# Optimization experiments

Hardware: AMD Instinct MI355X
Metric: run time of the kernel (lower is better)

## Reference

```python
import jax, jax.numpy as jnp
import numpy as np
from jax import lax

NUM_CLASSES = 80
CONF_THRESH = 0.05
NMS_THRESH = 0.6
TOPK = 2000          # topk_results per FPN level
IMG = 1280           # square input image
STRIDES = (8, 16, 32)
CLASS_OFFSET = 1.0e4 # > max box coordinate, for class-aware NMS offset trick


def setup_inputs() -> dict:
    key = jax.random.key(0)
    ks = jax.random.split(key, 6)
    inp = {}
    for i, s in enumerate(STRIDES):
        hw = (IMG // s) ** 2
        # classification logits; shift down so sigmoid scores are realistic
        inp[f"cls_p{i+3}"] = jax.random.normal(ks[i], (1, hw, NUM_CLASSES), jnp.float32) - 2.0
        # decoded boxes in absolute xyxy pixel coords
        u = jax.random.uniform(ks[i + 3], (1, hw, 4), jnp.float32)
        xy = u[..., :2] * (IMG - 260.0)
        wh = u[..., 2:] * 256.0 + 4.0
        inp[f"box_p{i+3}"] = jnp.concatenate([xy, xy + wh], axis=-1)
    inp["img_w"] = IMG
    inp["img_h"] = IMG
    return inp


def _box_iou(boxes):
    # boxes: [N,4] xyxy -> [N,N] IoU
    x1, y1, x2, y2 = boxes[:, 0], boxes[:, 1], boxes[:, 2], boxes[:, 3]
    area = jnp.maximum(x2 - x1, 0.0) * jnp.maximum(y2 - y1, 0.0)  # [N]
    lt = jnp.maximum(boxes[:, None, :2], boxes[None, :, :2])      # [N,N,2]
    rb = jnp.minimum(boxes[:, None, 2:], boxes[None, :, 2:])      # [N,N,2]
    wh = jnp.maximum(rb - lt, 0.0)
    inter = wh[..., 0] * wh[..., 1]
    union = area[:, None] + area[None, :] - inter
    return inter / jnp.maximum(union, 1e-9)


def _post_process(cls_list, box_list):
    all_scores, all_labels, all_boxes, all_valid = [], [], [], []
    for cls_i, box_i in zip(cls_list, box_list):
        cls0 = cls_i[0]                 # [HW, C]
        box0 = box_i[0]                 # [HW, 4]
        scores_flat = jax.nn.sigmoid(cls0).reshape(-1)      # [HW*C]
        k = min(TOPK, box0.shape[0])    # as in torch: min(topk_results, num_anchors)
        topk_scores, topk_idxs = lax.top_k(scores_flat, k)  # desc sort + take k
        valid = topk_scores > CONF_THRESH
        labels = topk_idxs % NUM_CLASSES
        anchor_idxs = topk_idxs // NUM_CLASSES
        all_scores.append(topk_scores)
        all_labels.append(labels)
        all_boxes.append(box0[anchor_idxs])
        all_valid.append(valid)
    scores = jnp.concatenate(all_scores)   # [N]
    labels = jnp.concatenate(all_labels)   # [N]
    boxes = jnp.concatenate(all_boxes)     # [N,4]
    valid = jnp.concatenate(all_valid)     # [N]

    # sort all candidates by score (invalid last)
    order = jnp.argsort(-jnp.where(valid, scores, -jnp.inf))
    scores, labels, boxes, valid = scores[order], labels[order], boxes[order], valid[order]

    # class-aware NMS (ca_nms=False): offset boxes per class so IoU across classes is 0
    off = labels.astype(boxes.dtype)[:, None] * CLASS_OFFSET
    iou = _box_iou(lax.stop_gradient(boxes + off))          # [N,N]

    n = scores.shape[0]
    idxr = jnp.arange(n)

    def body(i, st):
        keep, sup = st
        active = jnp.logical_not(sup[i])
        keep = keep.at[i].set(active)
        sup = sup | (active & (iou[i] > NMS_THRESH) & (idxr > i))
        return keep, sup

    keep, _ = lax.fori_loop(0, n, body, (jnp.zeros(n, bool), jnp.logical_not(valid)))
    return boxes, scores, labels, keep


def reference(cls_p3, cls_p4, cls_p5, box_p3, box_p4, box_p5, img_w, img_h):
    boxes, scores, labels, keep = _post_process(
        [cls_p3, cls_p4, cls_p5], [box_p3, box_p4, box_p5])
    scale = jnp.array([1.0 / img_w, 1.0 / img_h, 1.0 / img_w, 1.0 / img_h],
                      dtype=boxes.dtype)
    bboxes = jnp.clip(boxes * scale, 0.0, 1.0)
    # fixed-size padded result: `keep` marks the surviving detections
    return bboxes, scores, labels, keep
```

## Files before the change

### kernel.cpp

```cpp
#include <hip/hip_runtime.h>
#include <math.h>

#define L0T 2048000
#define L1T 512000
#define L2T 128000
#define LTOT 2688000
#define NTOT 5600
#define NW 88
#define NCB 2048
#define HB 128
#define CANDCAP 8192
#define LCHUNK 1024
#define GCHUNK 700
#define PAIRCAP 4096

__device__ __forceinline__ unsigned mkey(float f){
  unsigned u = __float_as_uint(f);
  return u ^ ((unsigned)(((int)u) >> 31) | 0x80000000u);
}

__global__ __launch_bounds__(256) void hist_blocks(const float* __restrict__ c0,
                                                   const float* __restrict__ c1,
                                                   const float* __restrict__ c2,
                                                   unsigned* __restrict__ blockHist){
  __shared__ unsigned lh[6 * NCB];
  for (int i = threadIdx.x; i < 6 * NCB; i += 256) lh[i] = 0;
  __syncthreads();
  int wv = threadIdx.x >> 6;
  unsigned* h0 = lh + wv * NCB;
  unsigned* h1 = lh + 4 * NCB;
  unsigned* h2 = lh + 5 * NCB;
  int g = blockIdx.x * 256 + threadIdx.x;
  const int Q = LTOT / 4;
  for (int q = g; q < Q; q += HB * 256){
    int e = q * 4;
    int idx; const float* p; unsigned* h;
    if (e < L0T){ idx = e; p = c0; h = h0; }
    else if (e < L0T + L1T){ idx = e - L0T; p = c1; h = h1; }
    else { idx = e - (L0T + L1T); p = c2; h = h2; }
    float4 v = *(const float4*)(p + idx);
    atomicAdd(&h[mkey(v.x) >> 21], 1u);
    atomicAdd(&h[mkey(v.y) >> 21], 1u);
    atomicAdd(&h[mkey(v.z) >> 21], 1u);
    atomicAdd(&h[mkey(v.w) >> 21], 1u);
  }
  __syncthreads();
  unsigned* out = blockHist + (size_t)blockIdx.x * 3 * NCB;
  for (int i = threadIdx.x; i < 3 * NCB; i += 256){
    unsigned s;
    if (i < NCB)            s = lh[i] + lh[NCB + i] + lh[2 * NCB + i] + lh[3 * NCB + i];
    else if (i < 2 * NCB)   s = lh[4 * NCB + (i - NCB)];
    else                    s = lh[5 * NCB + (i - 2 * NCB)];
    out[i] = s;
  }
}

__global__ __launch_bounds__(256) void reduce_hist24(const unsigned* __restrict__ blockHist,
                                                     unsigned* __restrict__ ghist){
  int c = blockIdx.x * 256 + threadIdx.x;
  unsigned s = 0;
#pragma unroll 8
  for (int b = 0; b < HB; ++b) s += blockHist[(size_t)b * 3 * NCB + c];
  ghist[c] = s;
}

__global__ __launch_bounds__(256) void threshbase_kernel(const unsigned* __restrict__ ghist,
                                                         const unsigned* __restrict__ blockHist,
                                                         unsigned* __restrict__ T,
                                                         unsigned* __restrict__ blockBase,
                                                         unsigned* __restrict__ candCnt){
  __shared__ unsigned h[NCB];
  __shared__ unsigned sT;
  __shared__ unsigned cb[HB];
  int lvl = blockIdx.x;
  for (int c = threadIdx.x; c < NCB; c += 256) h[c] = ghist[lvl * NCB + c];
  __syncthreads();
  if (threadIdx.x < 64){
    int lane = threadIdx.x;
    unsigned K = (lvl == 2) ? 1600u : 2000u;
    unsigned p = 0;
    for (int b = lane * 32; b < lane * 32 + 32; ++b) p += h[b];
    unsigned sincl = p;
    for (int d = 1; d < 64; d <<= 1){
      unsigned t = __shfl_down(sincl, d);
      if (lane + d < 64) sincl += t;
    }
    unsigned s_after = sincl - p;
    if (s_after < K && s_after + p >= K){
      unsigned acc = s_after;
      for (int b = lane * 32 + 31; b >= lane * 32; --b){
        acc += h[b];
        if (acc >= K){ sT = (unsigned)b; break; }
      }
    }
  }
  __syncthreads();
  unsigned tt = sT;
  if (threadIdx.x == 0) T[lvl] = tt;
  if (threadIdx.x < HB){
    const unsigned* bh = blockHist + (size_t)threadIdx.x * 3 * NCB + lvl * NCB;
    unsigned s = 0;
    for (unsigned c = tt; c < NCB; ++c) s += bh[c];
    cb[threadIdx.x] = s;
  }
  __syncthreads();
  if (threadIdx.x == 0){
    unsigned acc = 0;
    for (int b = 0; b < HB; ++b){ unsigned v = cb[b]; blockBase[lvl * HB + b] = acc; acc += v; }
    candCnt[lvl] = (acc > CANDCAP) ? CANDCAP : acc;
  }
}

__global__ __launch_bounds__(256) void compact_kernel(const float* __restrict__ c0,
                                                      const float* __restrict__ c1,
                                                      const float* __restrict__ c2,
                                                      const unsigned* __restrict__ T,
                                                      const unsigned* __restrict__ blockBase,
                                                      unsigned long long* __restrict__ cand){
  __shared__ unsigned run[3];
  if (threadIdx.x < 3) run[threadIdx.x] = 0;
  __syncthreads();
  unsigned t0 = T[0], t1 = T[1], t2 = T[2];
  unsigned bb0 = blockBase[0 * HB + blockIdx.x];
  unsigned bb1 = blockBase[1 * HB + blockIdx.x];
  unsigned bb2 = blockBase[2 * HB + blockIdx.x];
  int lane = threadIdx.x & 63;
  unsigned long long ltmask = (lane == 0) ? 0ull : ((1ull << lane) - 1ull);
  const int Q = LTOT / 4;
  for (int q = blockIdx.x * 256 + threadIdx.x; q < Q; q += HB * 256){
    int e = q * 4;
    int lvl, idx; const float* p; unsigned tt, bb;
    if (e < L0T){ lvl = 0; idx = e; p = c0; tt = t0; bb = bb0; }
    else if (e < L0T + L1T){ lvl = 1; idx = e - L0T; p = c1; tt = t1; bb = bb1; }
    else { lvl = 2; idx = e - (L0T + L1T); p = c2; tt = t2; bb = bb2; }
    float4 v = *(const float4*)(p + idx);
    unsigned k0 = mkey(v.x), k1 = mkey(v.y), k2 = mkey(v.z), k3 = mkey(v.w);
    bool p0 = (k0 >> 21) >= tt, p1 = (k1 >> 21) >= tt, p2 = (k2 >> 21) >= tt, p3 = (k3 >> 21) >= tt;
    unsigned long long bal0 = __ballot(p0), bal1 = __ballot(p1), bal2 = __ballot(p2), bal3 = __ballot(p3);
    unsigned n0 = (unsigned)__popcll(bal0), n1 = (unsigned)__popcll(bal1),
             n2 = (unsigned)__popcll(bal2), n3 = (unsigned)__popcll(bal3);
    unsigned wtot = n0 + n1 + n2 + n3;
    if (wtot == 0) continue;
    unsigned wold = 0;
    if (lane == 0) wold = atomicAdd(&run[lvl], wtot);
    wold = __shfl(wold, 0);
    unsigned base = bb + wold;
    if (p0){ unsigned pos = base + (unsigned)__popcll(bal0 & ltmask);
      if (pos < CANDCAP) cand[lvl * CANDCAP + pos] = ((unsigned long long)k0 << 32) | (unsigned)(~(unsigned)idx); }
    if (p1){ unsigned pos = base + n0 + (unsigned)__popcll(bal1 & ltmask);
      if (pos < CANDCAP) cand[lvl * CANDCAP + pos] = ((unsigned long long)k1 << 32) | (unsigned)(~(unsigned)(idx + 1)); }
    if (p2){ unsigned pos = base + n0 + n1 + (unsigned)__popcll(bal2 & ltmask);
      if (pos < CANDCAP) cand[lvl * CANDCAP + pos] = ((unsigned long long)k2 << 32) | (unsigned)(~(unsigned)(idx + 2)); }
    if (p3){ unsigned pos = base + n0 + n1 + n2 + (unsigned)__popcll(bal3 & ltmask);
      if (pos < CANDCAP) cand[lvl * CANDCAP + pos] = ((unsigned long long)k3 << 32) | (unsigned)(~(unsigned)(idx + 3)); }
  }
}

__global__ __launch_bounds__(256) void level_rank_partial(
    const unsigned* __restrict__ candCnt, const unsigned long long* __restrict__ cand,
    unsigned* __restrict__ lrank){
  __shared__ unsigned long long ch[LCHUNK];
  int lvl = blockIdx.z;
  int cnt = (int)candCnt[lvl];
  int j0 = blockIdx.y * LCHUNK;
  int i = blockIdx.x * 256 + threadIdx.x;
  if (j0 >= cnt || (int)(blockIdx.x * 256) >= cnt) return;
  int jn = cnt - j0; if (jn > LCHUNK) jn = LCHUNK;
  int jnP = (jn + 7) & ~7;
  for (int j = threadIdx.x; j < jn; j += 256) ch[j] = cand[lvl * CANDCAP + j0 + j];
  for (int j = jn + threadIdx.x; j < jnP; j += 256) ch[j] = 0ull;
  __syncthreads();
  if (i >= cnt) return;
  unsigned long long ki = cand[lvl * CANDCAP + i];
  int r0 = 0, r1 = 0, r2 = 0, r3 = 0;
  for (int j = 0; j < jnP; j += 8){
    unsigned long long a0 = ch[j+0], a1 = ch[j+1], a2 = ch[j+2], a3 = ch[j+3];
    unsigned long long a4 = ch[j+4], a5 = ch[j+5], a6 = ch[j+6], a7 = ch[j+7];
    r0 += (int)(a0 > ki) + (int)(a4 > ki);
    r1 += (int)(a1 > ki) + (int)(a5 > ki);
    r2 += (int)(a2 > ki) + (int)(a6 > ki);
    r3 += (int)(a3 > ki) + (int)(a7 > ki);
  }
  unsigned r = (unsigned)(r0 + r1 + r2 + r3);
  if (r) atomicAdd(&lrank[lvl * CANDCAP + i], r);
}

__global__ __launch_bounds__(256) void level_scatter(
    const float* __restrict__ box0, const float* __restrict__ box1, const float* __restrict__ box2,
    const unsigned* __restrict__ candCnt, const unsigned long long* __restrict__ cand,
    const unsigned* __restrict__ lrank,
    unsigned* __restrict__ ckey, float* __restrict__ cscore, int* __restrict__ clabel,
    float* __restrict__ cbox, unsigned* __restrict__ cvalid){
  int lvl = blockIdx.y;
  int cnt = (int)candCnt[lvl];
  int i = blockIdx.x * 256 + threadIdx.x;
  if (i >= cnt) return;
  unsigned K = (lvl == 2) ? 1600u : 2000u;
  unsigned r = lrank[lvl * CANDCAP + i];
  if (r >= K) return;
  const float* bx = (lvl == 0) ? box0 : ((lvl == 1) ? box1 : box2);
  unsigned long long ki = cand[lvl * CANDCAP + i];
  unsigned key = (unsigned)(ki >> 32);
  unsigned idxm = ~(unsigned)ki;
  int anchor = (int)(idxm / 80u);
  int lbl = (int)(idxm % 80u);
  unsigned fb = (key & 0x80000000u) ? (key ^ 0x80000000u) : ~key;
  float logit = __uint_as_float(fb);
  float sc = 1.0f / (1.0f + expf(-logit));
  int pos = lvl * 2000 + (int)r;
  ckey[pos] = key;
  cscore[pos] = sc;
  clabel[pos] = lbl;
  cvalid[pos] = (sc > 0.05f) ? 1u : 0u;
  float4 b = *(const float4*)(bx + (size_t)anchor * 4);
  *(float4*)(cbox + pos * 4) = b;
}

__global__ __launch_bounds__(256) void global_rank_partial(
    const unsigned* __restrict__ ckey, const unsigned* __restrict__ cvalid,
    unsigned* __restrict__ grank){
  __shared__ unsigned long long ch[GCHUNK + 4];
  int j0 = blockIdx.y * GCHUNK;
  for (int j = threadIdx.x; j < GCHUNK; j += 256){
    int g = j0 + j;
    unsigned eff = cvalid[g] ? ckey[g] : 0u;
    ch[j] = ((unsigned long long)eff << 32) | (unsigned)(~(unsigned)g);
  }
  if (threadIdx.x < 4) ch[GCHUNK + threadIdx.x] = 0ull;
  __syncthreads();
  int i = blockIdx.x * 256 + threadIdx.x;
  if (i >= NTOT) return;
  unsigned effi = cvalid[i] ? ckey[i] : 0u;
  unsigned long long ki = ((unsigned long long)effi << 32) | (unsigned)(~(unsigned)i);
  int r0 = 0, r1 = 0, r2 = 0, r3 = 0;
  for (int j = 0; j < GCHUNK + 4; j += 8){
    unsigned long long a0 = ch[j+0], a1 = ch[j+1], a2 = ch[j+2], a3 = ch[j+3];
    unsigned long long a4 = ch[j+4], a5 = ch[j+5], a6 = ch[j+6], a7 = ch[j+7];
    r0 += (int)(a0 > ki) + (int)(a4 > ki);
    r1 += (int)(a1 > ki) + (int)(a5 > ki);
    r2 += (int)(a2 > ki) + (int)(a6 > ki);
    r3 += (int)(a3 > ki) + (int)(a7 > ki);
  }
  unsigned r = (unsigned)(r0 + r1 + r2 + r3);
  if (r) atomicAdd(&grank[i], r);
}

__device__ __forceinline__ float read_dim(const int* p){
  int iv = p[0];
  if (iv > 0 && iv < (1 << 24)) return (float)iv;
  return __int_as_float(iv);
}

__global__ __launch_bounds__(256) void global_scatter(
    const unsigned* __restrict__ ckey, const float* __restrict__ cscore,
    const int* __restrict__ clabel, const float* __restrict__ cbox,
    const unsigned* __restrict__ cvalid, const unsigned* __restrict__ grank,
    const int* __restrict__ imw, const int* __restrict__ imh,
    float* __restrict__ out, int* __restrict__ slabel,
    float* __restrict__ soff, unsigned* __restrict__ svalid){
  int i = blockIdx.x * 256 + threadIdx.x;
  if (i >= NTOT) return;
  int r = (int)grank[i];
  int lbl = clabel[i];
  float off = (float)lbl * 10000.0f;
  slabel[r] = lbl;
  svalid[r] = cvalid[i];
  float4 b = *(const float4*)(cbox + (size_t)i * 4);
  float4 bo; bo.x = b.x + off; bo.y = b.y + off; bo.z = b.z + off; bo.w = b.w + off;
  *(float4*)(soff + (size_t)r * 4) = bo;
  float wv = read_dim(imw), hv = read_dim(imh);
  float sw = (float)(1.0 / (double)wv);
  float sh = (float)(1.0 / (double)hv);
  out[r * 4 + 0] = fminf(fmaxf(b.x * sw, 0.0f), 1.0f);
  out[r * 4 + 1] = fminf(fmaxf(b.y * sh, 0.0f), 1.0f);
  out[r * 4 + 2] = fminf(fmaxf(b.z * sw, 0.0f), 1.0f);
  out[r * 4 + 3] = fminf(fmaxf(b.w * sh, 0.0f), 1.0f);
  out[NTOT * 4 + r] = cscore[i];
  out[NTOT * 5 + r] = (float)lbl;
}

__global__ void nms_mask_kernel(const float* __restrict__ soff, const int* __restrict__ slabel,
                                unsigned* __restrict__ rowAny, unsigned long long* __restrict__ mask,
                                unsigned long long* __restrict__ diagT,
                                unsigned* __restrict__ pairsG, unsigned* __restrict__ pairCnt){
  __shared__ float cb[64][4];
  __shared__ float ca[64];
  __shared__ int cl[64];
  int wi = blockIdx.x, wj = blockIdx.y;
  if (wj < wi) return;
  int t = threadIdx.x;
  int i = wi * 64 + t;
  int j0 = wj * 64;
  int j = j0 + t;
  if (j < NTOT){
    float x1 = soff[j * 4 + 0], y1 = soff[j * 4 + 1];
    float x2 = soff[j * 4 + 2], y2 = soff[j * 4 + 3];
    cb[t][0] = x1; cb[t][1] = y1; cb[t][2] = x2; cb[t][3] = y2;
    {
#pragma clang fp contract(off)
      ca[t] = fmaxf(x2 - x1, 0.0f) * fmaxf(y2 - y1, 0.0f);
    }
    cl[t] = slabel[j];
  } else {
    cl[t] = -1;
  }
  __syncthreads();
  unsigned long long w = 0ull;
  if (i < NTOT){
    float ax1 = soff[i * 4 + 0], ay1 = soff[i * 4 + 1];
    float ax2 = soff[i * 4 + 2], ay2 = soff[i * 4 + 3];
    int li = slabel[i];
    float areaA;
    {
#pragma clang fp contract(off)
      areaA = fmaxf(ax2 - ax1, 0.0f) * fmaxf(ay2 - ay1, 0.0f);
    }
    for (int jj = 0; jj < 64; ++jj){
      int jg = j0 + jj;
      if (jg >= NTOT) break;
      if (jg <= i) continue;
      if (cl[jj] != li) continue;
      {
#pragma clang fp contract(off)
        float ltx = fmaxf(ax1, cb[jj][0]);
        float lty = fmaxf(ay1, cb[jj][1]);
        float rbx = fminf(ax2, cb[jj][2]);
        float rby = fminf(ay2, cb[jj][3]);
        float ww = fmaxf(rbx - ltx, 0.0f);
        float hh = fmaxf(rby - lty, 0.0f);
        float inter = ww * hh;
        float uni = (areaA + ca[jj]) - inter;
        float iou = inter / fmaxf(uni, 1e-9f);
        if (iou > 0.6f) w |= (1ull << jj);
      }
    }
    mask[(size_t)i * NW + wj] = w;
    if (w){
      rowAny[i] = 1u;
      int np = __popcll(w);
      unsigned base = atomicAdd(pairCnt, (unsigned)np);
      unsigned long long t2 = w; unsigned k = 0;
      while (t2){
        int b = __builtin_ctzll(t2); t2 &= t2 - 1;
        unsigned pos = base + k++;
        if (pos < PAIRCAP) pairsG[pos] = ((unsigned)i << 13) | (unsigned)(j0 + b);
      }
    }
  }
  if (wi == wj) diagT[wi * 64 + t] = w;
}

__global__ __launch_bounds__(256) void nms_scan_kernel(
    const unsigned long long* __restrict__ mask,
    const unsigned long long* __restrict__ diagT,
    const unsigned* __restrict__ rowAny,
    const unsigned* __restrict__ svalid,
    const unsigned* __restrict__ pairsG,
    const unsigned* __restrict__ pairCnt,
    float* __restrict__ out){
  __shared__ unsigned long long sdiag[NW * 64];
  __shared__ unsigned long long remW[NW];
  __shared__ unsigned long long keepL[NW];
  __shared__ unsigned long long activeW[NW];
  __shared__ unsigned spair[PAIRCAP];
  __shared__ unsigned bstart[NW];
  __shared__ unsigned bcnt[NW];
  __shared__ unsigned bcur[NW];
  int tid = threadIdx.x;
  int lane = tid & 63;
  int wv = tid >> 6;
  for (int i = tid; i < NW * 64; i += 256) sdiag[i] = diagT[i];
  for (int wd = wv; wd < NW; wd += 4){
    int e = wd * 64 + lane;
    unsigned a = (e < NTOT) ? rowAny[e] : 0u;
    unsigned v = (e < NTOT) ? svalid[e] : 0u;
    unsigned long long balv = __ballot(v != 0u);
    unsigned long long bala = __ballot(a != 0u && v != 0u);
    if (lane == 0){ remW[wd] = ~balv; activeW[wd] = bala; }
  }
  if (tid < NW) bcnt[tid] = 0;
  __syncthreads();
  unsigned np = *pairCnt;
  bool fast = (np <= PAIRCAP);
  if (fast){
    for (unsigned t = tid; t < np; t += 256) atomicAdd(&bcnt[pairsG[t] >> 19], 1u);
    __syncthreads();
    if (tid == 0){
      unsigned acc = 0;
      for (int b = 0; b < NW; ++b){ bstart[b] = acc; acc += bcnt[b]; }
    }
    if (tid < NW) bcur[tid] = 0;
    __syncthreads();
    for (unsigned t = tid; t < np; t += 256){
      unsigned pr = pairsG[t];
      unsigned b = pr >> 19;
      unsigned o = atomicAdd(&bcur[b], 1u);
      spair[bstart[b] + o] = pr;
    }
  }
  __syncthreads();
  if (wv == 0){
    if (fast){
      for (int c = 0; c < NW; ++c){
        unsigned long long rem = remW[c];
        unsigned long long D = sdiag[c * 64 + lane];
        unsigned long long nz = __ballot(D != 0ull);
        while (nz){
          int b = __builtin_ctzll(nz);
          nz &= nz - 1;
          unsigned long long Db = __shfl(D, b);
          if (!((rem >> b) & 1ull)) rem |= Db;
        }
        unsigned long long kp = ~rem;
        if (lane == 0) keepL[c] = kp;
        unsigned bs = bstart[c], bn = bcnt[c];
        for (unsigned t = lane; t < bn; t += 64){
          unsigned pr = spair[bs + t];
          unsigned ii = (pr >> 13) & 8191u;
          unsigned jj = pr & 8191u;
          if ((kp >> (ii & 63u)) & 1ull)
            atomicOr(&remW[jj >> 6], 1ull << (jj & 63u));
        }
        asm volatile("s_waitcnt lgkmcnt(0)" ::: "memory");
      }
    } else {
      unsigned long long rem0 = remW[lane];
      unsigned long long rem1 = (lane < NW - 64) ? remW[64 + lane] : ~0ull;
      for (int c = 0; c < NW; ++c){
        unsigned long long D = sdiag[c * 64 + lane];
        unsigned long long aw = activeW[c];
        unsigned long long a0 = __shfl(rem0, c & 63);
        unsigned long long a1 = __shfl(rem1, c & 63);
        unsigned long long rem = (c < 64) ? a0 : a1;
        unsigned long long nz = __ballot(D != 0ull);
        while (nz){
          int b = __builtin_ctzll(nz);
          nz &= nz - 1;
          unsigned long long Db = __shfl(D, b);
          if (!((rem >> b) & 1ull)) rem |= Db;
        }
        unsigned long long kp = ~rem;
        if (c < 64){ if (lane == c) rem0 = rem; }
        else       { if (lane == c - 64) rem1 = rem; }
        if (lane == 0) keepL[c] = kp;
        bool lo = (lane >= c);
        bool hi = (lane < NW - 64) && (64 + lane >= c);
        unsigned long long act = kp & aw;
        while (act){
          int b0 = __builtin_ctzll(act); act &= act - 1;
          const unsigned long long* p0 = mask + (size_t)(c * 64 + b0) * NW;
          unsigned long long l0a = lo ? p0[lane] : 0ull;
          unsigned long long l0b = hi ? p0[64 + lane] : 0ull;
          unsigned long long l1a = 0, l1b = 0, l2a = 0, l2b = 0, l3a = 0, l3b = 0;
          if (act){
            int b1 = __builtin_ctzll(act); act &= act - 1;
            const unsigned long long* p1 = mask + (size_t)(c * 64 + b1) * NW;
            l1a = lo ? p1[lane] : 0ull;
            l1b = hi ? p1[64 + lane] : 0ull;
            if (act){
              int b2 = __builtin_ctzll(act); act &= act - 1;
              const unsigned long long* p2 = mask + (size_t)(c * 64 + b2) * NW;
              l2a = lo ? p2[lane] : 0ull;
              l2b = hi ? p2[64 + lane] : 0ull;
              if (act){
                int b3 = __builtin_ctzll(act); act &= act - 1;
                const unsigned long long* p3 = mask + (size_t)(c * 64 + b3) * NW;
                l3a = lo ? p3[lane] : 0ull;
                l3b = hi ? p3[64 + lane] : 0ull;
              }
            }
          }
          rem0 |= l0a | l1a | l2a | l3a;
          rem1 |= l0b | l1b | l2b | l3b;
        }
      }
    }
  }
  __syncthreads();
  for (int r = tid; r < NTOT; r += 256)
    out[NTOT * 6 + r] = ((keepL[r >> 6] >> (r & 63)) & 1ull) ? 1.0f : 0.0f;
}

#define WS_TVAL      0u
#define WS_CANDCNT   16u
#define WS_ROWANY    32u
#define WS_PAIRCNT   22432u
#define WS_LRANK     22448u
#define WS_GRANK     120752u
#define WS_ZEROSZ    143120u
#define WS_BLOCKBASE 143152u
#define WS_GHIST     144688u
#define WS_PAIRS     169264u
#define WS_DIAGT     185648u
#define WS_CAND      230704u
#define WS_CKEY      427312u
#define WS_CSCORE    449712u
#define WS_CLABEL    472112u
#define WS_CBOX      494512u
#define WS_CVALID    584112u
#define WS_SLABEL    606512u
#define WS_SOFF      628912u
#define WS_SVALID    718512u
#define WS_MASK      740912u
#define WS_BLOCKHIST WS_MASK

extern "C" void kernel_launch(void* const* d_in, const int* in_sizes, int n_in,
                              void* d_out, int out_size, void* d_ws, size_t ws_size,
                              hipStream_t stream) {
  (void)in_sizes; (void)n_in; (void)out_size; (void)ws_size;
  const float* cls0 = (const float*)d_in[0];
  const float* box0 = (const float*)d_in[1];
  const float* cls1 = (const float*)d_in[2];
  const float* box1 = (const float*)d_in[3];
  const float* cls2 = (const float*)d_in[4];
  const float* box2 = (const float*)d_in[5];
  const int* imw = (const int*)d_in[6];
  const int* imh = (const int*)d_in[7];
  char* w = (char*)d_ws;
  unsigned* tval      = (unsigned*)(w + WS_TVAL);
  unsigned* candCnt   = (unsigned*)(w + WS_CANDCNT);
  unsigned* rowAny    = (unsigned*)(w + WS_ROWANY);
  unsigned* pairCnt   = (unsigned*)(w + WS_PAIRCNT);
  unsigned* lrank     = (unsigned*)(w + WS_LRANK);
  unsigned* grank     = (unsigned*)(w + WS_GRANK);
  unsigned* blockBase = (unsigned*)(w + WS_BLOCKBASE);
  unsigned* ghist     = (unsigned*)(w + WS_GHIST);
  unsigned* pairsG    = (unsigned*)(w + WS_PAIRS);
  unsigned long long* diagT = (unsigned long long*)(w + WS_DIAGT);
  unsigned long long* cand  = (unsigned long long*)(w + WS_CAND);
  unsigned* ckey   = (unsigned*)(w + WS_CKEY);
  float* cscore    = (float*)(w + WS_CSCORE);
  int* clabel      = (int*)(w + WS_CLABEL);
  float* cbox      = (float*)(w + WS_CBOX);
  unsigned* cvalid = (unsigned*)(w + WS_CVALID);
  int* slabel      = (int*)(w + WS_SLABEL);
  float* soff      = (float*)(w + WS_SOFF);
  unsigned* svalid = (unsigned*)(w + WS_SVALID);
  unsigned long long* mask  = (unsigned long long*)(w + WS_MASK);
  unsigned* blockHist = (unsigned*)(w + WS_BLOCKHIST);

  hipMemsetAsync(w + WS_ROWANY, 0, WS_ZEROSZ, stream);
  hist_blocks<<<HB, 256, 0, stream>>>(cls0, cls1, cls2, blockHist);
  reduce_hist24<<<24, 256, 0, stream>>>(blockHist, ghist);
  threshbase_kernel<<<3, 256, 0, stream>>>(ghist, blockHist, tval, blockBase, candCnt);
  compact_kernel<<<HB, 256, 0, stream>>>(cls0, cls1, cls2, tval, blockBase, cand);
  level_rank_partial<<<dim3(32, 8, 3), 256, 0, stream>>>(candCnt, cand, lrank);
  level_scatter<<<dim3(32, 3), 256, 0, stream>>>(box0, box1, box2, candCnt, cand, lrank,
                                                 ckey, cscore, clabel, cbox, cvalid);
  global_rank_partial<<<dim3(22, 8), 256, 0, stream>>>(ckey, cvalid, grank);
  global_scatter<<<22, 256, 0, stream>>>(ckey, cscore, clabel, cbox, cvalid, grank,
                                         imw, imh, (float*)d_out, slabel, soff, svalid);
  nms_mask_kernel<<<dim3(88, 88), 64, 0, stream>>>(soff, slabel, rowAny, mask, diagT,
                                                   pairsG, pairCnt);
  nms_scan_kernel<<<1, 256, 0, stream>>>(mask, diagT, rowAny, svalid, pairsG, pairCnt,
                                         (float*)d_out);
}
```

Measured before the change: 229.4 us.

## Replace sequential NMS pair scan with parallel fixed-point iteration; spread histogram atomics

The fast NMS path no longer runs a single wave block-by-block over 88 words with diagonal resolution. It now iterates a parallel fixed point: every pass, all threads apply the suppression pairs from the currently kept boxes, and it stops once the keep mask no longer changes. This trades a serial dependency chain for repeated full passes, whose count depends on how long the suppression chains are. Separately, the histogram kernel spreads level-0 and level-1 atomics across lane-indexed sub-histograms to reduce LDS atomic contention. It also skips loading the diagonal tiles when the fast path is taken.

```diff
diff --git a/kernel.cpp b/kernel.cpp
--- a/kernel.cpp
+++ b/kernel.cpp
@@ -23,13 +23,12 @@
                                                    const float* __restrict__ c1,
                                                    const float* __restrict__ c2,
                                                    unsigned* __restrict__ blockHist){
-  __shared__ unsigned lh[6 * NCB];
-  for (int i = threadIdx.x; i < 6 * NCB; i += 256) lh[i] = 0;
-  __syncthreads();
-  int wv = threadIdx.x >> 6;
-  unsigned* h0 = lh + wv * NCB;
-  unsigned* h1 = lh + 4 * NCB;
-  unsigned* h2 = lh + 5 * NCB;
+  __shared__ unsigned lh[7 * NCB];
+  for (int i = threadIdx.x; i < 7 * NCB; i += 256) lh[i] = 0;
+  __syncthreads();
+  unsigned* h0 = lh + (threadIdx.x & 3) * NCB;
+  unsigned* h1 = lh + (4 + (threadIdx.x & 1)) * NCB;
+  unsigned* h2 = lh + 6 * NCB;
   int g = blockIdx.x * 256 + threadIdx.x;
   const int Q = LTOT / 4;
   for (int q = g; q < Q; q += HB * 256){
@@ -48,9 +47,9 @@
   unsigned* out = blockHist + (size_t)blockIdx.x * 3 * NCB;
   for (int i = threadIdx.x; i < 3 * NCB; i += 256){
     unsigned s;
-    if (i < NCB)            s = lh[i] + lh[NCB + i] + lh[2 * NCB + i] + lh[3 * NCB + i];
-    else if (i < 2 * NCB)   s = lh[4 * NCB + (i - NCB)];
-    else                    s = lh[5 * NCB + (i - 2 * NCB)];
+    if (i < NCB)          s = lh[i] + lh[NCB + i] + lh[2 * NCB + i] + lh[3 * NCB + i];
+    else if (i < 2 * NCB) s = lh[4 * NCB + (i - NCB)] + lh[5 * NCB + (i - NCB)];
+    else                  s = lh[6 * NCB + (i - 2 * NCB)];
     out[i] = s;
   }
 }
@@ -359,73 +358,57 @@
     const unsigned* __restrict__ pairCnt,
     float* __restrict__ out){
   __shared__ unsigned long long sdiag[NW * 64];
-  __shared__ unsigned long long remW[NW];
-  __shared__ unsigned long long keepL[NW];
+  __shared__ unsigned long long validW[NW];
+  __shared__ unsigned long long keepW[NW];
   __shared__ unsigned long long activeW[NW];
+  __shared__ unsigned supW[NW * 2];
   __shared__ unsigned spair[PAIRCAP];
-  __shared__ unsigned bstart[NW];
-  __shared__ unsigned bcnt[NW];
-  __shared__ unsigned bcur[NW];
+  __shared__ int schanged;
   int tid = threadIdx.x;
   int lane = tid & 63;
   int wv = tid >> 6;
-  for (int i = tid; i < NW * 64; i += 256) sdiag[i] = diagT[i];
   for (int wd = wv; wd < NW; wd += 4){
     int e = wd * 64 + lane;
     unsigned a = (e < NTOT) ? rowAny[e] : 0u;
     unsigned v = (e < NTOT) ? svalid[e] : 0u;
     unsigned long long balv = __ballot(v != 0u);
     unsigned long long bala = __ballot(a != 0u && v != 0u);
-    if (lane == 0){ remW[wd] = ~balv; activeW[wd] = bala; }
-  }
-  if (tid < NW) bcnt[tid] = 0;
+    if (lane == 0){ validW[wd] = balv; activeW[wd] = bala; }
+  }
   __syncthreads();
   unsigned np = *pairCnt;
   bool fast = (np <= PAIRCAP);
   if (fast){
-    for (unsigned t = tid; t < np; t += 256) atomicAdd(&bcnt[pairsG[t] >> 19], 1u);
+    for (unsigned t = tid; t < np; t += 256) spair[t] = pairsG[t];
+    if (tid < NW) keepW[tid] = validW[tid];
     __syncthreads();
-    if (tid == 0){
-      unsigned acc = 0;
-      for (int b = 0; b < NW; ++b){ bstart[b] = acc; acc += bcnt[b]; }
-    }
-    if (tid < NW) bcur[tid] = 0;
+    for (int pass = 0; pass < PAIRCAP; ++pass){
+      if (tid < NW){ supW[2 * tid] = 0u; supW[2 * tid + 1] = 0u; }
+      if (tid == 0) schanged = 0;
+      __syncthreads();
+      for (unsigned t = tid; t < np; t += 256){
+        unsigned pr = spair[t];
+        unsigned ii = pr >> 13;
+        unsigned jj = pr & 8191u;
+        if ((keepW[ii >> 6] >> (ii & 63u)) & 1ull)
+          atomicOr(&supW[jj >> 5], 1u << (jj & 31u));
+      }
+      __syncthreads();
+      if (tid < NW){
+        unsigned long long sup = (unsigned long long)supW[2 * tid] |
+                                 ((unsigned long long)supW[2 * tid + 1] << 32);
+        unsigned long long nk = validW[tid] & ~sup;
+        if (nk != keepW[tid]){ keepW[tid] = nk; schanged = 1; }
+      }
+      __syncthreads();
+      if (!schanged) break;
+    }
+  } else {
+    for (int i = tid; i < NW * 64; i += 256) sdiag[i] = diagT[i];
     __syncthreads();
-    for (unsigned t = tid; t < np; t += 256){
-      unsigned pr = pairsG[t];
-      unsigned b = pr >> 19;
-      unsigned o = atomicAdd(&bcur[b], 1u);
-      spair[bstart[b] + o] = pr;
-    }
-  }
-  __syncthreads();
-  if (wv == 0){
-    if (fast){
-      for (int c = 0; c < NW; ++c){
-        unsigned long long rem = remW[c];
-        unsigned long long D = sdiag[c * 64 + lane];
-        unsigned long long nz = __ballot(D != 0ull);
-        while (nz){
-          int b = __builtin_ctzll(nz);
-          nz &= nz - 1;
-          unsigned long long Db = __shfl(D, b);
-          if (!((rem >> b) & 1ull)) rem |= Db;
-        }
-        unsigned long long kp = ~rem;
-        if (lane == 0) keepL[c] = kp;
-        unsigned bs = bstart[c], bn = bcnt[c];
-        for (unsigned t = lane; t < bn; t += 64){
-          unsigned pr = spair[bs + t];
-          unsigned ii = (pr >> 13) & 8191u;
-          unsigned jj = pr & 8191u;
-          if ((kp >> (ii & 63u)) & 1ull)
-            atomicOr(&remW[jj >> 6], 1ull << (jj & 63u));
-        }
-        asm volatile("s_waitcnt lgkmcnt(0)" ::: "memory");
-      }
-    } else {
-      unsigned long long rem0 = remW[lane];
-      unsigned long long rem1 = (lane < NW - 64) ? remW[64 + lane] : ~0ull;
+    if (wv == 0){
+      unsigned long long rem0 = ~validW[lane];
+      unsigned long long rem1 = (lane < NW - 64) ? ~validW[64 + lane] : ~0ull;
       for (int c = 0; c < NW; ++c){
         unsigned long long D = sdiag[c * 64 + lane];
         unsigned long long aw = activeW[c];
@@ -442,7 +425,7 @@
         unsigned long long kp = ~rem;
         if (c < 64){ if (lane == c) rem0 = rem; }
         else       { if (lane == c - 64) rem1 = rem; }
-        if (lane == 0) keepL[c] = kp;
+        if (lane == 0) keepW[c] = kp;
         bool lo = (lane >= c);
         bool hi = (lane < NW - 64) && (64 + lane >= c);
         unsigned long long act = kp & aw;
@@ -478,7 +461,7 @@
   }
   __syncthreads();
   for (int r = tid; r < NTOT; r += 256)
-    out[NTOT * 6 + r] = ((keepL[r >> 6] >> (r & 63)) & 1ull) ? 1.0f : 0.0f;
+    out[NTOT * 6 + r] = ((keepW[r >> 6] >> (r & 63)) & 1ull) ? 1.0f : 0.0f;
 }
 
 #define WS_TVAL      0u
```

Result: faster. 206.8 us (-9.9%).
